# Kernel tuning notes

Hardware: AMD Instinct MI355X
Metric: run time of the kernel (lower is better)

The kernel has to match this reference:

```python
import jax, jax.numpy as jnp
import numpy as np

K = 7            # pool_size / PSROI_BINS
FEAT_STRIDE = 4
SAMPLES = 2      # bilinear sampling points per bin side (RoIAlign-style avg)


def setup_inputs() -> dict:
    key = jax.random.key(0)
    ks = jax.random.split(key, 4)
    B, H, W, C = 1, 200, 304, 4 * K * K  # C = k*k*dim, dim=4
    features = jax.random.normal(ks[0], (B, H, W, C), jnp.float32)
    Himg, Wimg = H * FEAT_STRIDE, W * FEAT_STRIDE
    N = 512
    u = jax.random.uniform(ks[1], (N, 4), jnp.float32)
    x1 = u[:, 0] * (Wimg - 64.0)
    y1 = u[:, 1] * (Himg - 64.0)
    x2 = jnp.minimum(x1 + 32.0 + u[:, 2] * (Wimg / 4.0), Wimg - 1.0)
    y2 = jnp.minimum(y1 + 32.0 + u[:, 3] * (Himg / 4.0), Himg - 1.0)
    rois = jnp.stack([x1, y1, x2, y2], axis=-1)  # (N,4) image coords
    W_off = jax.random.normal(ks[2], (3, 3, C, 2 * C), jnp.float32) * 0.01
    b_off = jnp.zeros((2 * C,), jnp.float32)
    return {"features": features, "rois": rois, "W_off": W_off, "b_off": b_off}


def _deform_sample(x, off):
    # x: (B,H,W,C); off: (B,H,W,C,2) as (dy,dx) per channel.
    B, H, W, C = x.shape
    gy = jnp.arange(H, dtype=x.dtype)[None, :, None, None]
    gx = jnp.arange(W, dtype=x.dtype)[None, None, :, None]
    yy = jnp.clip(gy + off[..., 0], 0.0, H - 1.0)
    xx = jnp.clip(gx + off[..., 1], 0.0, W - 1.0)
    y0 = jnp.floor(yy); x0 = jnp.floor(xx)
    wy = yy - y0; wx = xx - x0
    y0i = y0.astype(jnp.int32); x0i = x0.astype(jnp.int32)
    y1i = jnp.minimum(y0i + 1, H - 1); x1i = jnp.minimum(x0i + 1, W - 1)
    bi = jnp.arange(B)[:, None, None, None]
    ci = jnp.arange(C)[None, None, None, :]
    v00 = x[bi, y0i, x0i, ci]; v01 = x[bi, y0i, x1i, ci]
    v10 = x[bi, y1i, x0i, ci]; v11 = x[bi, y1i, x1i, ci]
    top = v00 + (v01 - v00) * wx
    bot = v10 + (v11 - v10) * wx
    return top + (bot - top) * wy


def _ps_roi(fm, rois):
    # fm: (H,W,C) offset feature map; rois: (N,4) image coords (x1,y1,x2,y2).
    H, W, C = fm.shape
    dim = C // (K * K)
    fmg = fm.reshape(H, W, K * K, dim)  # position-sensitive channel groups
    b = rois / jnp.asarray(FEAT_STRIDE, fm.dtype)
    x1, y1, x2, y2 = b[:, 0], b[:, 1], b[:, 2], b[:, 3]
    bh = (y2 - y1) / K; bw = (x2 - x1) / K  # per-roi bin sizes (N,)
    i = jnp.arange(K, dtype=fm.dtype)
    s = (jnp.arange(SAMPLES, dtype=fm.dtype) + 0.5) / SAMPLES
    sy = y1[:, None, None] + (i[None, :, None] + s[None, None, :]) * bh[:, None, None]
    sx = x1[:, None, None] + (i[None, :, None] + s[None, None, :]) * bw[:, None, None]
    yy = jnp.clip(sy, 0.0, H - 1.0)[:, :, None, :, None]  # (N,Ki,1,S,1)
    xx = jnp.clip(sx, 0.0, W - 1.0)[:, None, :, None, :]  # (N,1,Kj,1,S)
    y0 = jnp.floor(yy); wy = (yy - y0)[..., None]
    x0 = jnp.floor(xx); wx = (xx - x0)[..., None]
    y0i = y0.astype(jnp.int32); y1i = jnp.minimum(y0i + 1, H - 1)
    x0i = x0.astype(jnp.int32); x1i = jnp.minimum(x0i + 1, W - 1)
    g = (jnp.arange(K)[:, None] * K + jnp.arange(K)[None, :])[None, :, :, None, None]
    v00 = fmg[y0i, x0i, g, :]; v01 = fmg[y0i, x1i, g, :]  # (N,K,K,S,S,dim)
    v10 = fmg[y1i, x0i, g, :]; v11 = fmg[y1i, x1i, g, :]
    top = v00 + (v01 - v00) * wx
    bot = v10 + (v11 - v10) * wx
    vals = top + (bot - top) * wy
    return vals.mean(axis=(3, 4))  # (N,K,K,dim)


def reference(features, rois, W_off, b_off):
    B, H, W, C = features.shape
    offs = jax.lax.conv_general_dilated(
        features, W_off, (1, 1), "SAME",
        dimension_numbers=("NHWC", "HWIO", "NHWC")) + b_off  # (B,H,W,2C)
    off = offs.reshape(B, H, W, C, 2)
    offset_map = _deform_sample(features, off)  # deformable offset resampling
    return _ps_roi(offset_map[0], rois)
```

## Files before the change

### kernel.cpp

```cpp
#include <hip/hip_runtime.h>


constexpr int H = 200, W = 304, C = 196, CO = 392;
constexpr int KK = 7, DIM = 4, NROI = 512;
constexpr int KW = 224;
constexpr int KP = 232;
constexpr size_t F_ELEMS = (size_t)H * W * KW;
constexpr size_t W_ELEMS = (size_t)49 * 9 * 8 * KW;
constexpr size_t WS_NEED = (F_ELEMS + W_ELEMS) * 2;

typedef __attribute__((ext_vector_type(8))) short bf16x8;
typedef __attribute__((ext_vector_type(4))) float f32x4;

static __device__ inline unsigned short f2bf(float x) {
  unsigned int u = __float_as_uint(x);
  return (unsigned short)((u + 0x7FFFu + ((u >> 16) & 1u)) >> 16);
}

static __device__ inline void roi_geom(const float* __restrict__ rois, int n,
                                       int bi, int bj,
                                       int* ycand, int* xcand,
                                       float* wy, float* wx) {
  const float rx1 = rois[n * 4 + 0] * 0.25f;
  const float ry1 = rois[n * 4 + 1] * 0.25f;
  const float rx2 = rois[n * 4 + 2] * 0.25f;
  const float ry2 = rois[n * 4 + 3] * 0.25f;
  const float bh = (ry2 - ry1) * (1.0f / 7.0f);
  const float bw = (rx2 - rx1) * (1.0f / 7.0f);
#pragma unroll
  for (int si = 0; si < 2; ++si) {
    float sy = ry1 + ((float)bi + ((float)si + 0.5f) * 0.5f) * bh;
    sy = fminf(fmaxf(sy, 0.0f), (float)(H - 1));
    float fy = floorf(sy);
    wy[si] = sy - fy;
    int i0 = (int)fy;
    ycand[2 * si] = i0;
    ycand[2 * si + 1] = min(i0 + 1, H - 1);

    float sx = rx1 + ((float)bj + ((float)si + 0.5f) * 0.5f) * bw;
    sx = fminf(fmaxf(sx, 0.0f), (float)(W - 1));
    float fx = floorf(sx);
    wx[si] = sx - fx;
    int j0 = (int)fx;
    xcand[2 * si] = j0;
    xcand[2 * si + 1] = min(j0 + 1, W - 1);
  }
}

__global__ __launch_bounds__(256) void fprep_kernel(
    const float* __restrict__ feat, unsigned short* __restrict__ fbf)
{
  const long long u = (long long)blockIdx.x * 256 + threadIdx.x;
  const long long TOT = (long long)H * W * (KW / 4);
  if (u >= TOT) return;
  const int k4 = (int)(u % (KW / 4));
  const long long pix = u / (KW / 4);
  const int k = k4 * 4;
  ushort4 v = make_ushort4(0, 0, 0, 0);
  const float* src = feat + pix * C;
#pragma unroll
  for (int j = 0; j < 4; ++j)
    if (k + j < C) ((unsigned short*)&v)[j] = f2bf(src[k + j]);
  *reinterpret_cast<ushort4*>(fbf + pix * KW + k) = v;
}

__global__ __launch_bounds__(256) void wprep_kernel(
    const float* __restrict__ Woff, unsigned short* __restrict__ wbf)
{
  const int u = blockIdx.x * 256 + threadIdx.x;
  const int TOT = 49 * 9 * 8 * (KW / 4);
  if (u >= TOT) return;
  const int k4 = u % (KW / 4);
  const int n  = (u / (KW / 4)) % 8;
  const int p  = (u / (KW / 4 * 8)) % 9;
  const int g  = u / (KW / 4 * 8 * 9);
  const int k  = k4 * 4;
  ushort4 v = make_ushort4(0, 0, 0, 0);
  const int o = g * 8 + n;
#pragma unroll
  for (int j = 0; j < 4; ++j)
    if (k + j < C)
      ((unsigned short*)&v)[j] = f2bf(Woff[(size_t)(p * C + k + j) * CO + o]);
  *reinterpret_cast<ushort4*>(wbf + ((size_t)(g * 9 + p) * 8 + n) * KW + k) = v;
}

__global__ __launch_bounds__(256) void psroi_direct_kernel(
    const float* __restrict__ feat, const float* __restrict__ rois,
    const unsigned short* __restrict__ fbf,
    const unsigned short* __restrict__ wbf,
    const float* __restrict__ boff, float* __restrict__ out)
{
  const int bid = blockIdx.x;
  const int wid = (bid & 7) * (49 * NROI / 4 / 8) + (bid >> 3);
  const int wv = threadIdx.x >> 6;
  const int lane = threadIdx.x & 63;
  const int site = wid * 4 + wv;
  const int n = site / 49, g = site % 49;
  const int bi = g / KK, bj = g % KK;
  const int m_lane = lane & 15;
  const int k_hi = lane >> 4;

  __shared__ float Cw[4][16][9];

  int yc4[4], xc4[4];
  float wy2[2], wx2[2];
  roi_geom(rois, n, bi, bj, yc4, xc4, wy2, wx2);

  const int ycc = yc4[m_lane >> 2];
  const int xcc = xc4[m_lane & 3];

  f32x4 acc = {0.f, 0.f, 0.f, 0.f};

#pragma unroll 1
  for (int p = 0; p < 9; ++p) {
    const int dy = p / 3 - 1, dx = p % 3 - 1;
    const int ys = ycc + dy, xs = xcc + dx;
    const bool valid = (ys >= 0) && (ys < H) && (xs >= 0) && (xs < W);
    const unsigned short* arow = fbf + (size_t)(ys * W + xs) * KW + k_hi * 8;
    const unsigned short* brow =
        wbf + ((size_t)(g * 9 + p) * 8 + m_lane) * KW + k_hi * 8;
    const bool bval = (m_lane < 8);
#pragma unroll
    for (int ks = 0; ks < 7; ++ks) {
      bf16x8 a = (bf16x8)(short)0;
      if (valid) a = *reinterpret_cast<const bf16x8*>(arow + ks * 32);
      bf16x8 b = (bf16x8)(short)0;
      if (bval) b = *reinterpret_cast<const bf16x8*>(brow + ks * 32);
      acc = __builtin_amdgcn_mfma_f32_16x16x32_bf16(a, b, acc, 0, 0, 0);
    }
  }

  if (m_lane < 8) {
#pragma unroll
    for (int r = 0; r < 4; ++r)
      Cw[wv][k_hi * 4 + r][m_lane] = acc[r];
  }
  __syncthreads();

  {
    const int corner = lane >> 2;
    const int d = lane & 3;
    const int yc = yc4[corner >> 2];
    const int xc = xc4[corner & 3];
    const int c = g * DIM + d;

    const float offy = Cw[wv][corner][2 * d]     + boff[2 * c];
    const float offx = Cw[wv][corner][2 * d + 1] + boff[2 * c + 1];

    float yy = fminf(fmaxf((float)yc + offy, 0.0f), (float)(H - 1));
    float xx = fminf(fmaxf((float)xc + offx, 0.0f), (float)(W - 1));
    const float fy = floorf(yy), fx = floorf(xx);
    const float ay = yy - fy, ax = xx - fx;
    const int iy0 = (int)fy, ix0 = (int)fx;
    const int iy1 = min(iy0 + 1, H - 1), ix1 = min(ix0 + 1, W - 1);
    const float v00 = feat[(size_t)(iy0 * W + ix0) * C + c];
    const float v01 = feat[(size_t)(iy0 * W + ix1) * C + c];
    const float v10 = feat[(size_t)(iy1 * W + ix0) * C + c];
    const float v11 = feat[(size_t)(iy1 * W + ix1) * C + c];
    const float top = v00 + (v01 - v00) * ax;
    const float bot = v10 + (v11 - v10) * ax;
    const float om = top + (bot - top) * ay;

    const int yci = corner >> 2, xci = corner & 3;
    const int si = yci >> 1, a = yci & 1;
    const int sj = xci >> 1, b = xci & 1;
    const float cy = a ? wy2[si] : 1.0f - wy2[si];
    const float cx = b ? wx2[sj] : 1.0f - wx2[sj];
    float v = 0.25f * cy * cx * om;

    v += __shfl_xor(v, 4);
    v += __shfl_xor(v, 8);
    v += __shfl_xor(v, 16);
    v += __shfl_xor(v, 32);

    if (lane < 4)
      out[(size_t)n * (KK * KK * DIM) + g * DIM + lane] = v;
  }
}

__global__ __launch_bounds__(256) void psroi_union_kernel(
    const float* __restrict__ feat, const float* __restrict__ rois,
    const float* __restrict__ Woff, const float* __restrict__ boff,
    float* __restrict__ out)
{
  const int bid = blockIdx.x;
  const int wid = (bid & 7) * (49 * NROI / 8) + (bid >> 3);
  const int g = wid % 49;
  const int n = wid / 49;
  const int bi = g / KK, bj = g % KK;
  const int tid = threadIdx.x;
  const int lane = tid & 63;
  const int wv = tid >> 6;
  const int m_lane = lane & 15;
  const int k_hi = lane >> 4;

  __shared__ short Abuf[64 * KP];
  __shared__ float Cbuf[4 * 16 * 9];

  for (int i = tid; i < 64 * (KP - C); i += 256) {
    const int row = i / (KP - C), col = C + i % (KP - C);
    Abuf[row * KP + col] = 0;
  }

  int yc4[4], xc4[4];
  float wy2[2], wx2[2];
  roi_geom(rois, n, bi, bj, yc4, xc4, wy2, wx2);

  {
    const int pos = tid >> 2;
    const int yi = pos >> 3, xi = pos & 7;
    const int yrow = (yi < 4) ? (yc4[0] + yi - 1) : (yc4[2] + yi - 5);
    const int xcol = (xi < 4) ? (xc4[0] + xi - 1) : (xc4[2] + xi - 5);
    const bool valid = (yrow >= 0) && (yrow < H) && (xcol >= 0) && (xcol < W);
    const float* frow = feat + (size_t)(yrow * W + xcol) * C;
    short* arow = &Abuf[pos * KP];
    const int l = tid & 3;
#pragma unroll
    for (int k = 0; k <= 12; ++k) {
      const int c = l + 4 * k;
      if (c < 49) {
        ushort4 v = make_ushort4(0, 0, 0, 0);
        if (valid) {
          const float4 f4 = *reinterpret_cast<const float4*>(frow + 4 * c);
          v.x = f2bf(f4.x); v.y = f2bf(f4.y);
          v.z = f2bf(f4.z); v.w = f2bf(f4.w);
        }
        *reinterpret_cast<ushort4*>(arow + 4 * c) = v;
      }
    }
  }
  __syncthreads();

  const int i0 = m_lane >> 2, j0 = m_lane & 3;
  const int dyA = yc4[1] - yc4[0], dyB = yc4[3] - yc4[2];
  const int dxA = xc4[1] - xc4[0], dxB = xc4[3] - xc4[2];
  int ybase = (i0 & 2) ? 5 : 1;
  ybase += (i0 & 1) ? ((i0 & 2) ? dyB : dyA) : 0;
  int xbase = (j0 & 2) ? 5 : 1;
  xbase += (j0 & 1) ? ((j0 & 2) ? dxB : dxA) : 0;

  f32x4 acc = {0.f, 0.f, 0.f, 0.f};

#pragma unroll 1
  for (int p = wv; p < 9; p += 4) {
    bf16x8 bfr[7];
#pragma unroll
    for (int ks = 0; ks < 7; ++ks) bfr[ks] = (bf16x8)(short)0;
    if (m_lane < 8) {
#pragma unroll
      for (int ks = 0; ks < 7; ++ks) {
        bf16x8 b = (bf16x8)(short)0;
#pragma unroll
        for (int j = 0; j < 8; ++j) {
          const int k = ks * 32 + k_hi * 8 + j;
          if (k < C)
            b[j] = (short)f2bf(Woff[(size_t)(p * C + k) * CO + g * 8 + m_lane]);
        }
        bfr[ks] = b;
      }
    }
    const int row = (ybase + p / 3 - 1) * 8 + (xbase + p % 3 - 1);
    const short* arow = &Abuf[row * KP];
#pragma unroll
    for (int ks = 0; ks < 7; ++ks) {
      const bf16x8 a = *reinterpret_cast<const bf16x8*>(arow + ks * 32 + k_hi * 8);
      acc = __builtin_amdgcn_mfma_f32_16x16x32_bf16(a, bfr[ks], acc, 0, 0, 0);
    }
  }

  if (m_lane < 8) {
#pragma unroll
    for (int r = 0; r < 4; ++r)
      Cbuf[(wv * 16 + k_hi * 4 + r) * 9 + m_lane] = acc[r];
  }
  __syncthreads();

  if (tid < 64) {
    const int corner = tid >> 2;
    const int d = tid & 3;
    const int yc = yc4[corner >> 2];
    const int xc = xc4[corner & 3];
    const int c = g * DIM + d;

    float offy = boff[2 * c], offx = boff[2 * c + 1];
#pragma unroll
    for (int w = 0; w < 4; ++w) {
      offy += Cbuf[(w * 16 + corner) * 9 + 2 * d];
      offx += Cbuf[(w * 16 + corner) * 9 + 2 * d + 1];
    }

    float yy = fminf(fmaxf((float)yc + offy, 0.0f), (float)(H - 1));
    float xx = fminf(fmaxf((float)xc + offx, 0.0f), (float)(W - 1));
    const float fy = floorf(yy), fx = floorf(xx);
    const float ay = yy - fy, ax = xx - fx;
    const int iy0 = (int)fy, ix0 = (int)fx;
    const int iy1 = min(iy0 + 1, H - 1), ix1 = min(ix0 + 1, W - 1);
    const float v00 = feat[(size_t)(iy0 * W + ix0) * C + c];
    const float v01 = feat[(size_t)(iy0 * W + ix1) * C + c];
    const float v10 = feat[(size_t)(iy1 * W + ix0) * C + c];
    const float v11 = feat[(size_t)(iy1 * W + ix1) * C + c];
    const float top = v00 + (v01 - v00) * ax;
    const float bot = v10 + (v11 - v10) * ax;
    const float om = top + (bot - top) * ay;

    const int yci = corner >> 2, xci = corner & 3;
    const int si = yci >> 1, a = yci & 1;
    const int sj = xci >> 1, b = xci & 1;
    const float cy = a ? wy2[si] : 1.0f - wy2[si];
    const float cx = b ? wx2[sj] : 1.0f - wx2[sj];
    float v = 0.25f * cy * cx * om;

    v += __shfl_xor(v, 4);
    v += __shfl_xor(v, 8);
    v += __shfl_xor(v, 16);
    v += __shfl_xor(v, 32);

    if (tid < 4)
      out[(size_t)n * (KK * KK * DIM) + g * DIM + tid] = v;
  }
}

extern "C" void kernel_launch(void* const* d_in, const int* in_sizes, int n_in,
                              void* d_out, int out_size, void* d_ws, size_t ws_size,
                              hipStream_t stream) {
  const float* feat = (const float*)d_in[0];
  const float* rois = (const float*)d_in[1];
  const float* Woff = (const float*)d_in[2];
  const float* boff = (const float*)d_in[3];
  float* out = (float*)d_out;

  if (ws_size >= WS_NEED) {
    unsigned short* fbf = (unsigned short*)d_ws;
    unsigned short* wbf = fbf + F_ELEMS;
    const long long ftot = (long long)H * W * (KW / 4);
    fprep_kernel<<<dim3((unsigned)((ftot + 255) / 256)), dim3(256), 0, stream>>>(
        feat, fbf);
    const int wtot = 49 * 9 * 8 * (KW / 4);
    wprep_kernel<<<dim3((wtot + 255) / 256), dim3(256), 0, stream>>>(Woff, wbf);
    psroi_direct_kernel<<<dim3(49 * NROI / 4), dim3(256), 0, stream>>>(
        feat, rois, fbf, wbf, boff, out);
  } else {
    psroi_union_kernel<<<dim3(49 * NROI), dim3(256), 0, stream>>>(
        feat, rois, Woff, boff, out);
  }
}
```

Baseline: 240.8 us.

## Stage 8x8 bf16 feature patch in LDS and split 3x3 taps across waves

Replaces the one-wave-per-site direct kernel with one block per (roi, bin) site. The block cooperatively loads the 8x8 neighborhood patch of bf16 features into padded LDS, and the four waves split the nine conv taps, reading A operands from LDS. Partial sums are then reduced through shared memory. This cuts redundant global loads of overlapping 3x3 neighborhoods, at the cost of four times more blocks, a larger LDS footprint and extra synchronisation.

```diff
diff --git a/kernel.cpp b/kernel.cpp
--- a/kernel.cpp
+++ b/kernel.cpp
@@ -4,6 +4,7 @@
 constexpr int H = 200, W = 304, C = 196, CO = 392;
 constexpr int KK = 7, DIM = 4, NROI = 512;
 constexpr int KW = 224;
+constexpr int KP2 = 242;
 constexpr int KP = 232;
 constexpr size_t F_ELEMS = (size_t)H * W * KW;
 constexpr size_t W_ELEMS = (size_t)49 * 9 * 8 * KW;
@@ -84,68 +85,102 @@
   *reinterpret_cast<ushort4*>(wbf + ((size_t)(g * 9 + p) * 8 + n) * KW + k) = v;
 }
 
-__global__ __launch_bounds__(256) void psroi_direct_kernel(
+__global__ __launch_bounds__(256) void psroi_union8_kernel(
     const float* __restrict__ feat, const float* __restrict__ rois,
     const unsigned short* __restrict__ fbf,
     const unsigned short* __restrict__ wbf,
     const float* __restrict__ boff, float* __restrict__ out)
 {
   const int bid = blockIdx.x;
-  const int wid = (bid & 7) * (49 * NROI / 4 / 8) + (bid >> 3);
-  const int wv = threadIdx.x >> 6;
-  const int lane = threadIdx.x & 63;
-  const int site = wid * 4 + wv;
-  const int n = site / 49, g = site % 49;
+  const int wid = (bid & 7) * (49 * NROI / 8) + (bid >> 3);
+  const int g = wid % 49;
+  const int n = wid / 49;
   const int bi = g / KK, bj = g % KK;
+  const int tid = threadIdx.x;
+  const int lane = tid & 63;
+  const int wv = tid >> 6;
   const int m_lane = lane & 15;
   const int k_hi = lane >> 4;
 
-  __shared__ float Cw[4][16][9];
+  __shared__ __align__(16) short Abuf[64 * KP2];
 
   int yc4[4], xc4[4];
   float wy2[2], wx2[2];
   roi_geom(rois, n, bi, bj, yc4, xc4, wy2, wx2);
 
-  const int ycc = yc4[m_lane >> 2];
-  const int xcc = xc4[m_lane & 3];
+  {
+    const int pos = tid >> 2;
+    const int yi = pos >> 3, xi = pos & 7;
+    const int yrow = (yi < 4) ? (yc4[0] + yi - 1) : (yc4[2] + yi - 5);
+    const int xcol = (xi < 4) ? (xc4[0] + xi - 1) : (xc4[2] + xi - 5);
+    const bool valid = (yrow >= 0) && (yrow < H) && (xcol >= 0) && (xcol < W);
+    const unsigned short* frow = fbf + (size_t)(yrow * W + xcol) * KW;
+    short* arow = &Abuf[pos * KP2];
+    const int l = tid & 3;
+#pragma unroll
+    for (int k = 0; k < 7; ++k) {
+      const int c = l + 4 * k;
+      bf16x8 v = (bf16x8)(short)0;
+      if (valid) v = *reinterpret_cast<const bf16x8*>(frow + c * 8);
+      *reinterpret_cast<bf16x8*>(arow + c * 8) = v;
+    }
+  }
+  __syncthreads();
+
+  const int i0 = m_lane >> 2, j0 = m_lane & 3;
+  const int dyA = yc4[1] - yc4[0], dyB = yc4[3] - yc4[2];
+  const int dxA = xc4[1] - xc4[0], dxB = xc4[3] - xc4[2];
+  int ybase = (i0 & 2) ? 5 : 1;
+  ybase += (i0 & 1) ? ((i0 & 2) ? dyB : dyA) : 0;
+  int xbase = (j0 & 2) ? 5 : 1;
+  xbase += (j0 & 1) ? ((j0 & 2) ? dxB : dxA) : 0;
 
   f32x4 acc = {0.f, 0.f, 0.f, 0.f};
 
 #pragma unroll 1
-  for (int p = 0; p < 9; ++p) {
-    const int dy = p / 3 - 1, dx = p % 3 - 1;
-    const int ys = ycc + dy, xs = xcc + dx;
-    const bool valid = (ys >= 0) && (ys < H) && (xs >= 0) && (xs < W);
-    const unsigned short* arow = fbf + (size_t)(ys * W + xs) * KW + k_hi * 8;
-    const unsigned short* brow =
-        wbf + ((size_t)(g * 9 + p) * 8 + m_lane) * KW + k_hi * 8;
-    const bool bval = (m_lane < 8);
+  for (int p = wv; p < 9; p += 4) {
+    bf16x8 bfr[7];
+#pragma unroll
+    for (int ks = 0; ks < 7; ++ks) bfr[ks] = (bf16x8)(short)0;
+    if (m_lane < 8) {
+      const unsigned short* wrow =
+          wbf + ((size_t)(g * 9 + p) * 8 + m_lane) * KW + k_hi * 8;
+#pragma unroll
+      for (int ks = 0; ks < 7; ++ks)
+        bfr[ks] = *reinterpret_cast<const bf16x8*>(wrow + ks * 32);
+    }
+
+    const int row = (ybase + p / 3 - 1) * 8 + (xbase + p % 3 - 1);
+    const short* arow = &Abuf[row * KP2];
 #pragma unroll
     for (int ks = 0; ks < 7; ++ks) {
-      bf16x8 a = (bf16x8)(short)0;
-      if (valid) a = *reinterpret_cast<const bf16x8*>(arow + ks * 32);
-      bf16x8 b = (bf16x8)(short)0;
-      if (bval) b = *reinterpret_cast<const bf16x8*>(brow + ks * 32);
-      acc = __builtin_amdgcn_mfma_f32_16x16x32_bf16(a, b, acc, 0, 0, 0);
-    }
-  }
-
+      const bf16x8 a = *reinterpret_cast<const bf16x8*>(arow + ks * 32 + k_hi * 8);
+      acc = __builtin_amdgcn_mfma_f32_16x16x32_bf16(a, bfr[ks], acc, 0, 0, 0);
+    }
+  }
+
+  __syncthreads();
+  float* Cst = reinterpret_cast<float*>(Abuf);
   if (m_lane < 8) {
 #pragma unroll
     for (int r = 0; r < 4; ++r)
-      Cw[wv][k_hi * 4 + r][m_lane] = acc[r];
-  }
-  __syncthreads();
-
-  {
-    const int corner = lane >> 2;
-    const int d = lane & 3;
+      Cst[(wv * 16 + k_hi * 4 + r) * 9 + m_lane] = acc[r];
+  }
+  __syncthreads();
+
+  if (tid < 64) {
+    const int corner = tid >> 2;
+    const int d = tid & 3;
     const int yc = yc4[corner >> 2];
     const int xc = xc4[corner & 3];
     const int c = g * DIM + d;
 
-    const float offy = Cw[wv][corner][2 * d]     + boff[2 * c];
-    const float offx = Cw[wv][corner][2 * d + 1] + boff[2 * c + 1];
+    float offy = boff[2 * c], offx = boff[2 * c + 1];
+#pragma unroll
+    for (int w = 0; w < 4; ++w) {
+      offy += Cst[(w * 16 + corner) * 9 + 2 * d];
+      offx += Cst[(w * 16 + corner) * 9 + 2 * d + 1];
+    }
 
     float yy = fminf(fmaxf((float)yc + offy, 0.0f), (float)(H - 1));
     float xx = fminf(fmaxf((float)xc + offx, 0.0f), (float)(W - 1));
@@ -173,8 +208,8 @@
     v += __shfl_xor(v, 16);
     v += __shfl_xor(v, 32);
 
-    if (lane < 4)
-      out[(size_t)n * (KK * KK * DIM) + g * DIM + lane] = v;
+    if (tid < 4)
+      out[(size_t)n * (KK * KK * DIM) + g * DIM + tid] = v;
   }
 }
 
@@ -337,7 +372,7 @@
         feat, fbf);
     const int wtot = 49 * 9 * 8 * (KW / 4);
     wprep_kernel<<<dim3((wtot + 255) / 256), dim3(256), 0, stream>>>(Woff, wbf);
-    psroi_direct_kernel<<<dim3(49 * NROI / 4), dim3(256), 0, stream>>>(
+    psroi_union8_kernel<<<dim3(49 * NROI), dim3(256), 0, stream>>>(
         feat, rois, fbf, wbf, boff, out);
   } else {
     psroi_union_kernel<<<dim3(49 * NROI), dim3(256), 0, stream>>>(
```

After: 278.8 us. 15.8% more time.
